# Performance work log

Hardware: AMD Instinct MI355X
Metric: run time of the kernel (lower is better)

Reference implementation:

```python
import jax, jax.numpy as jnp
import numpy as np

SPARSE_SHAPE = (41, 1600, 1408)  # (D, H, W), batch_size = 1
N_VOXELS = 200000
BN_EPS = 1e-3


def _kernel_offsets():
    # 27 offsets of a 3x3x3 kernel, padding=1 -> offsets in {-1,0,1}^3
    g = np.stack(np.meshgrid(*([np.arange(-1, 2)] * 3), indexing='ij'), axis=-1)
    return jnp.asarray(g.reshape(-1, 3), dtype=jnp.int32)  # (27, 3)


def _neighbor_map(coords):
    """Submanifold rulebook: for each active voxel and each of 27 offsets,
    index of the active neighbor voxel, or N (sentinel) if inactive/out-of-bounds."""
    D, H, W = SPARSE_SHAPE
    N = coords.shape[0]
    b, z, y, x = coords[:, 0], coords[:, 1], coords[:, 2], coords[:, 3]
    flat = ((b * D + z) * H + y) * W + x  # batch_size=1
    grid = jnp.full((D * H * W,), N, dtype=jnp.int32).at[flat].set(
        jnp.arange(N, dtype=jnp.int32))
    offs = _kernel_offsets()                      # (27, 3)
    nc = coords[:, None, 1:4] + offs[None]        # (N, 27, 3)
    lim = jnp.asarray([D, H, W], dtype=jnp.int32)
    valid = jnp.all((nc >= 0) & (nc < lim), axis=-1)  # (N, 27)
    nflat = ((b[:, None] * D + nc[..., 0]) * H + nc[..., 1]) * W + nc[..., 2]
    nbr = jnp.where(valid, grid[jnp.where(valid, nflat, 0)], N)
    return nbr  # (N, 27) int32, sentinel = N


def _subm_conv(features, nbr, w):
    # gather -> batched small GEMM -> (implicit) scatter back to same voxels
    pad = jnp.concatenate(
        [features, jnp.zeros((1, features.shape[1]), features.dtype)], axis=0)
    gathered = pad[nbr]                           # (N, 27, Cin)
    return jnp.einsum('nkc,kcd->nd', gathered, w)  # (N, Cout)


def _bn_relu(x, gamma, beta):
    # BatchNorm1d in train mode over the voxel (batch) dim, eps=1e-3
    mean = x.mean(axis=0)
    var = x.var(axis=0)
    return jax.nn.relu((x - mean) * jax.lax.rsqrt(var + BN_EPS) * gamma + beta)


def setup_inputs() -> dict:
    D, H, W = SPARSE_SHAPE
    total = D * H * W
    rng = np.random.default_rng(0)
    # unique active voxel locations
    flat = np.unique(rng.integers(0, total, size=N_VOXELS + 20000))
    rng.shuffle(flat)
    flat = flat[:N_VOXELS]
    assert flat.shape[0] == N_VOXELS
    z = flat // (H * W)
    y = (flat // W) % H
    x = flat % W
    b = np.zeros_like(z)
    coords = jnp.asarray(np.stack([b, z, y, x], axis=1), dtype=jnp.int32)

    key = jax.random.key(0)
    k0, k1, k2 = jax.random.split(key, 3)
    features = jax.random.uniform(k0, (N_VOXELS, 3), dtype=jnp.float32)
    w1 = jax.random.normal(k1, (27, 3, 16), dtype=jnp.float32) * 0.1
    w2 = jax.random.normal(k2, (27, 16, 16), dtype=jnp.float32) * 0.05
    return {
        'features': features, 'coords': coords,
        'w1': w1, 'gamma1': jnp.ones(16, jnp.float32), 'beta1': jnp.zeros(16, jnp.float32),
        'w2': w2, 'gamma2': jnp.ones(16, jnp.float32), 'beta2': jnp.zeros(16, jnp.float32),
    }


def reference(features, coords, w1, gamma1, beta1, w2, gamma2, beta2):
    nbr = _neighbor_map(coords)   # shared indice_key='subm1' -> reused by both convs
    h = _bn_relu(_subm_conv(features, nbr, w1), gamma1, beta1)
    h = _bn_relu(_subm_conv(h, nbr, w2), gamma2, beta2)
    return h
```

## Files before the change

kernel.cpp:

```cpp
#include <hip/hip_runtime.h>
#include <stdint.h>

#define SPARSE_D 41
#define SPARSE_H 1600
#define SPARSE_W 1408
#define BN_EPS 0.001f

static constexpr int NYB = SPARSE_H / 2;
static constexpr int NBUCKET = SPARSE_D * NYB;
static constexpr int PCAP = 12;


__global__ void k_insert(const int* __restrict__ coords, uint32_t* __restrict__ bent, int N) {
    int n = blockIdx.x * blockDim.x + threadIdx.x;
    if (n >= N) return;
    int4 c4 = ((const int4*)coords)[n];
    int z = c4.y, y = c4.z, x = c4.w;
    int b = z * NYB + (y >> 1);
    uint32_t e = ((uint32_t)(y & 1) << 29) | ((uint32_t)x << 18) | (uint32_t)n;
    int slot = atomicAdd((int*)&bent[(size_t)b * 32], 1) + 1;
    if (slot <= 31) bent[(size_t)b * 32 + slot] = e;
}

__device__ __forceinline__ void stats_epilogue(const float acc[16],
                                               float* __restrict__ partials,
                                               float (*sred)[32]) {
    int lid = threadIdx.x & 63;
    int wid = threadIdx.x >> 6;
    #pragma unroll
    for (int d = 0; d < 16; ++d) {
        float v = acc[d];
        float v2 = v * v;
        #pragma unroll
        for (int off = 32; off; off >>= 1) {
            v += __shfl_xor(v, off);
            v2 += __shfl_xor(v2, off);
        }
        if (lid == 0) { sred[wid][d] = v; sred[wid][16 + d] = v2; }
    }
    __syncthreads();
    if (threadIdx.x < 32)
        partials[(size_t)blockIdx.x * 32 + threadIdx.x] =
            sred[0][threadIdx.x] + sred[1][threadIdx.x] +
            sred[2][threadIdx.x] + sred[3][threadIdx.x];
}

__global__ void k_build_conv1(const int* __restrict__ coords, const uint32_t* __restrict__ bent,
                              const float* __restrict__ feat, const float* __restrict__ w1,
                              int* __restrict__ pcnt, uint32_t* __restrict__ pairs,
                              float* __restrict__ h1, float* __restrict__ partials, int N) {
    __shared__ float sred[4][32];
    int n = blockIdx.x * blockDim.x + threadIdx.x;
    float acc[16];
    #pragma unroll
    for (int d = 0; d < 16; ++d) acc[d] = 0.f;
    if (n < N) {
        int4 c4 = ((const int4*)coords)[n];
        int z = c4.y, y = c4.z, x = c4.w;

        float f0 = feat[n * 3 + 0], f1 = feat[n * 3 + 1], f2 = feat[n * 3 + 2];
        const float* wd = w1 + 13 * 48;
        #pragma unroll
        for (int d = 0; d < 16; ++d)
            acc[d] = fmaf(f0, wd[d], fmaf(f1, wd[16 + d], f2 * wd[32 + d]));

        int yb0 = (y - 1) >> 1;
        uint4 q0[6];
        int bix[6], mm[6];
        #pragma unroll
        for (int p = 0; p < 6; ++p) {
            int zz = z + p / 2 - 1;
            int yb = yb0 + (p & 1);
            bool v = ((unsigned)zz < SPARSE_D) & ((unsigned)yb < NYB);
            int b = v ? (zz * NYB + yb) : 0;
            bix[p] = b;
            q0[p] = *(const uint4*)&bent[(size_t)b * 32];
            mm[p] = v ? 1 : 0;
        }

        uint32_t lpairs[PCAP];
        int cnt = 0;
        #pragma unroll
        for (int p = 0; p < 6; ++p) {
            int m = mm[p] ? min((int)q0[p].x, 31) : 0;
            int yb = yb0 + (p & 1);
            int dzk = (p / 2) * 9;
            auto scan_entry = [&](uint32_t e, int slot) {
                if (slot > m) return;
                int ey = (yb << 1) + (int)(e >> 29);
                int ex = (int)((e >> 18) & 0x7FFu);
                int dy = ey - y, dx = ex - x;
                if ((unsigned)(dy + 1) > 2u || (unsigned)(dx + 1) > 2u) return;
                uint32_t idx = e & 0x3FFFFu;
                if (idx == (uint32_t)n) return;
                int k = dzk + (dy + 1) * 3 + (dx + 1);
                if (cnt < PCAP) lpairs[cnt] = ((uint32_t)k << 18) | idx;
                ++cnt;
            };
            scan_entry(q0[p].y, 1);
            scan_entry(q0[p].z, 2);
            scan_entry(q0[p].w, 3);
            for (int w = 4; w <= m; w += 4) {
                uint4 q = *(const uint4*)&bent[(size_t)bix[p] * 32 + w];
                scan_entry(q.x, w);
                scan_entry(q.y, w + 1);
                scan_entry(q.z, w + 2);
                scan_entry(q.w, w + 3);
            }
        }
        cnt = min(cnt, PCAP);
        pcnt[n] = cnt;
        for (int c = 0; c < cnt; ++c) {
            uint32_t pr = lpairs[c];
            pairs[(size_t)c * N + n] = pr;
            int k = (int)(pr >> 18), idx = (int)(pr & 0x3FFFFu);
            float g0 = feat[idx * 3 + 0], g1 = feat[idx * 3 + 1], g2 = feat[idx * 3 + 2];
            const float* wk = w1 + k * 48;
            #pragma unroll
            for (int d = 0; d < 16; ++d)
                acc[d] = fmaf(g0, wk[d], fmaf(g1, wk[16 + d], fmaf(g2, wk[32 + d], acc[d])));
        }
        float4* o = (float4*)&h1[(size_t)n * 16];
        o[0] = make_float4(acc[0], acc[1], acc[2], acc[3]);
        o[1] = make_float4(acc[4], acc[5], acc[6], acc[7]);
        o[2] = make_float4(acc[8], acc[9], acc[10], acc[11]);
        o[3] = make_float4(acc[12], acc[13], acc[14], acc[15]);
    }
    stats_epilogue(acc, partials, sred);
}

__global__ void k_conv2(const float* __restrict__ h1, const int* __restrict__ pcnt,
                        const uint32_t* __restrict__ pairs, const float* __restrict__ w2,
                        const float* __restrict__ scsh1, float* __restrict__ out,
                        float* __restrict__ partials, int N) {
    __shared__ float sred[4][32];
    __shared__ float sc[16], sh[16];
    if (threadIdx.x < 16) { sc[threadIdx.x] = scsh1[threadIdx.x]; sh[threadIdx.x] = scsh1[16 + threadIdx.x]; }
    __syncthreads();
    int n = blockIdx.x * blockDim.x + threadIdx.x;
    float acc[16];
    #pragma unroll
    for (int d = 0; d < 16; ++d) acc[d] = 0.f;
    if (n < N) {
        float g[16];
        #pragma unroll
        for (int c = 0; c < 16; c += 4) {
            float4 t = *(const float4*)&h1[(size_t)n * 16 + c];
            g[c]     = fmaxf(fmaf(t.x, sc[c],     sh[c]),     0.f);
            g[c + 1] = fmaxf(fmaf(t.y, sc[c + 1], sh[c + 1]), 0.f);
            g[c + 2] = fmaxf(fmaf(t.z, sc[c + 2], sh[c + 2]), 0.f);
            g[c + 3] = fmaxf(fmaf(t.w, sc[c + 3], sh[c + 3]), 0.f);
        }
        {
            const float* w = w2 + 13 * 256;
            #pragma unroll
            for (int c = 0; c < 16; ++c)
                #pragma unroll
                for (int d = 0; d < 16; ++d)
                    acc[d] = fmaf(g[c], w[c * 16 + d], acc[d]);
        }
        int m = min(pcnt[n], PCAP);
        for (int cc = 0; cc < m; ++cc) {
            uint32_t pr = pairs[(size_t)cc * N + n];
            int k = (int)(pr >> 18), idx = (int)(pr & 0x3FFFFu);
            #pragma unroll
            for (int c = 0; c < 16; c += 4) {
                float4 t = *(const float4*)&h1[(size_t)idx * 16 + c];
                g[c]     = fmaxf(fmaf(t.x, sc[c],     sh[c]),     0.f);
                g[c + 1] = fmaxf(fmaf(t.y, sc[c + 1], sh[c + 1]), 0.f);
                g[c + 2] = fmaxf(fmaf(t.z, sc[c + 2], sh[c + 2]), 0.f);
                g[c + 3] = fmaxf(fmaf(t.w, sc[c + 3], sh[c + 3]), 0.f);
            }
            const float* wk = w2 + k * 256;
            #pragma unroll
            for (int c = 0; c < 16; ++c)
                #pragma unroll
                for (int d = 0; d < 16; ++d)
                    acc[d] = fmaf(g[c], wk[c * 16 + d], acc[d]);
        }
        float4* o = (float4*)&out[(size_t)n * 16];
        o[0] = make_float4(acc[0], acc[1], acc[2], acc[3]);
        o[1] = make_float4(acc[4], acc[5], acc[6], acc[7]);
        o[2] = make_float4(acc[8], acc[9], acc[10], acc[11]);
        o[3] = make_float4(acc[12], acc[13], acc[14], acc[15]);
    }
    stats_epilogue(acc, partials, sred);
}

__global__ void k_finalize(const float* __restrict__ partials, int nb,
                           const float* __restrict__ gamma, const float* __restrict__ beta,
                           float* __restrict__ scsh, float invN) {
    __shared__ float red[32][33];
    int ch = threadIdx.x & 31;
    int rg = threadIdx.x >> 5;
    float s0 = 0.f, s1 = 0.f, s2 = 0.f, s3 = 0.f;
    int j = rg;
    for (; j + 96 < nb; j += 128) {
        s0 += partials[(size_t)(j      ) * 32 + ch];
        s1 += partials[(size_t)(j + 32 ) * 32 + ch];
        s2 += partials[(size_t)(j + 64 ) * 32 + ch];
        s3 += partials[(size_t)(j + 96 ) * 32 + ch];
    }
    for (; j < nb; j += 32) s0 += partials[(size_t)j * 32 + ch];
    red[rg][ch] = (s0 + s1) + (s2 + s3);
    __syncthreads();
    if (threadIdx.x < 32) {
        float t = 0.f;
        #pragma unroll
        for (int r = 0; r < 32; ++r) t += red[r][threadIdx.x];
        red[0][threadIdx.x] = t;
    }
    __syncthreads();
    if (threadIdx.x < 16) {
        int d = threadIdx.x;
        float mean = red[0][d] * invN;
        float var = red[0][16 + d] * invN - mean * mean;
        float s2c = gamma[d] * rsqrtf(var + BN_EPS);
        scsh[d] = s2c;
        scsh[16 + d] = beta[d] - mean * s2c;
    }
}

__global__ void k_bnrelu4(float* __restrict__ x, const float* __restrict__ scsh, int nvec) {
    __shared__ float sc[16], sh[16];
    if (threadIdx.x < 16) { sc[threadIdx.x] = scsh[threadIdx.x]; sh[threadIdx.x] = scsh[16 + threadIdx.x]; }
    __syncthreads();
    int i = blockIdx.x * blockDim.x + threadIdx.x;
    if (i < nvec) {
        float4 v = ((float4*)x)[i];
        int c0 = (i & 3) * 4;
        v.x = fmaxf(fmaf(v.x, sc[c0 + 0], sh[c0 + 0]), 0.f);
        v.y = fmaxf(fmaf(v.y, sc[c0 + 1], sh[c0 + 1]), 0.f);
        v.z = fmaxf(fmaf(v.z, sc[c0 + 2], sh[c0 + 2]), 0.f);
        v.w = fmaxf(fmaf(v.w, sc[c0 + 3], sh[c0 + 3]), 0.f);
        ((float4*)x)[i] = v;
    }
}

extern "C" void kernel_launch(void* const* d_in, const int* in_sizes, int n_in,
                              void* d_out, int out_size, void* d_ws, size_t ws_size,
                              hipStream_t stream) {
    const float* feat   = (const float*)d_in[0];
    const int*   coords = (const int*)d_in[1];
    const float* w1     = (const float*)d_in[2];
    const float* gamma1 = (const float*)d_in[3];
    const float* beta1  = (const float*)d_in[4];
    const float* w2     = (const float*)d_in[5];
    const float* gamma2 = (const float*)d_in[6];
    const float* beta2  = (const float*)d_in[7];
    float* out = (float*)d_out;
    const int N = in_sizes[0] / 3;

    const int T = 256;
    const int nb = (N + T - 1) / T;
    const int nvec = N * 16 / 4;
    const int nbv = (nvec + T - 1) / T;

    char* ws = (char*)d_ws;
    size_t off = 0;
    uint32_t* bent = (uint32_t*)(ws + off);  off += (size_t)NBUCKET * 32 * 4;
    int* pcnt = (int*)(ws + off);            off += ((size_t)N * 4 + 63) & ~(size_t)63;
    uint32_t* pairs = (uint32_t*)(ws + off); off += (size_t)PCAP * N * 4;
    float* h1 = (float*)(ws + off);          off += (size_t)N * 16 * 4;
    float* partials = (float*)(ws + off);    off += ((size_t)nb * 32 * 4 + 63) & ~(size_t)63;
    float* stats = (float*)(ws + off);

    hipMemsetAsync(bent, 0, (size_t)NBUCKET * 32 * 4, stream);
    k_insert<<<nb, T, 0, stream>>>(coords, bent, N);
    k_build_conv1<<<nb, T, 0, stream>>>(coords, bent, feat, w1, pcnt, pairs, h1, partials, N);
    k_finalize<<<1, 1024, 0, stream>>>(partials, nb, gamma1, beta1, stats, 1.f / (float)N);
    k_conv2<<<nb, T, 0, stream>>>(h1, pcnt, pairs, w2, stats, out, partials, N);
    k_finalize<<<1, 1024, 0, stream>>>(partials, nb, gamma2, beta2, stats + 32, 1.f / (float)N);
    k_bnrelu4<<<nbv, T, 0, stream>>>(out, stats + 32, nvec);
}
```

Before: 154.5 us.

## Fuse second BN finalize into apply kernel, pack pair count, stage outputs via LDS

The second finalize kernel is folded into the final BN+ReLU kernel. Each of its 128 persistent blocks now reduces the partials redundantly and then applies the result with a grid-stride loop, which removes one launch. The per-voxel pair count is packed into the top bits of the first pair word, dropping the separate pcnt array and one load. h1 and out writes, plus the self-row read of h1 in conv2, go through a shared-memory staging buffer so global accesses are fully coalesced float4s. In exchange it adds 16KB of LDS per block and extra barriers, and h1 is padded to a whole number of blocks.

```diff
diff --git a/kernel.cpp b/kernel.cpp
--- a/kernel.cpp
+++ b/kernel.cpp
@@ -45,11 +45,48 @@
             sred[2][threadIdx.x] + sred[3][threadIdx.x];
 }
 
+__device__ __forceinline__ void reduce_scsh(const float* __restrict__ partials, int nbp,
+                                            const float* __restrict__ gamma,
+                                            const float* __restrict__ beta,
+                                            float invN, float (*red)[33],
+                                            float* __restrict__ scsh) {
+    int ch = threadIdx.x & 31;
+    int rg = threadIdx.x >> 5;
+    float s0 = 0.f, s1 = 0.f, s2 = 0.f, s3 = 0.f;
+    int j = rg;
+    for (; j + 24 < nbp; j += 32) {
+        s0 += partials[(size_t)(j     ) * 32 + ch];
+        s1 += partials[(size_t)(j +  8) * 32 + ch];
+        s2 += partials[(size_t)(j + 16) * 32 + ch];
+        s3 += partials[(size_t)(j + 24) * 32 + ch];
+    }
+    for (; j < nbp; j += 8) s0 += partials[(size_t)j * 32 + ch];
+    red[rg][ch] = (s0 + s1) + (s2 + s3);
+    __syncthreads();
+    if (threadIdx.x < 32) {
+        float t = 0.f;
+        #pragma unroll
+        for (int r = 0; r < 8; ++r) t += red[r][threadIdx.x];
+        red[0][threadIdx.x] = t;
+    }
+    __syncthreads();
+    if (threadIdx.x < 16) {
+        int d = threadIdx.x;
+        float mean = red[0][d] * invN;
+        float var  = red[0][16 + d] * invN - mean * mean;
+        float sc = gamma[d] * rsqrtf(var + BN_EPS);
+        scsh[d] = sc;
+        scsh[16 + d] = beta[d] - mean * sc;
+    }
+    __syncthreads();
+}
+
 __global__ void k_build_conv1(const int* __restrict__ coords, const uint32_t* __restrict__ bent,
                               const float* __restrict__ feat, const float* __restrict__ w1,
-                              int* __restrict__ pcnt, uint32_t* __restrict__ pairs,
+                              uint32_t* __restrict__ pairs,
                               float* __restrict__ h1, float* __restrict__ partials, int N) {
     __shared__ float sred[4][32];
+    __shared__ float4 stage[256 * 4];
     int n = blockIdx.x * blockDim.x + threadIdx.x;
     float acc[16];
     #pragma unroll
@@ -109,10 +146,10 @@
             }
         }
         cnt = min(cnt, PCAP);
-        pcnt[n] = cnt;
+        pairs[n] = ((uint32_t)cnt << 24) | (cnt ? (lpairs[0] & 0xFFFFFFu) : 0u);
+        for (int c = 1; c < cnt; ++c) pairs[(size_t)c * N + n] = lpairs[c];
         for (int c = 0; c < cnt; ++c) {
             uint32_t pr = lpairs[c];
-            pairs[(size_t)c * N + n] = pr;
             int k = (int)(pr >> 18), idx = (int)(pr & 0x3FFFFu);
             float g0 = feat[idx * 3 + 0], g1 = feat[idx * 3 + 1], g2 = feat[idx * 3 + 2];
             const float* wk = w1 + k * 48;
@@ -120,22 +157,71 @@
             for (int d = 0; d < 16; ++d)
                 acc[d] = fmaf(g0, wk[d], fmaf(g1, wk[16 + d], fmaf(g2, wk[32 + d], acc[d])));
         }
-        float4* o = (float4*)&h1[(size_t)n * 16];
-        o[0] = make_float4(acc[0], acc[1], acc[2], acc[3]);
-        o[1] = make_float4(acc[4], acc[5], acc[6], acc[7]);
-        o[2] = make_float4(acc[8], acc[9], acc[10], acc[11]);
-        o[3] = make_float4(acc[12], acc[13], acc[14], acc[15]);
-    }
+    }
+    #pragma unroll
+    for (int r = 0; r < 4; ++r)
+        stage[threadIdx.x * 4 + r] = make_float4(acc[r * 4], acc[r * 4 + 1],
+                                                 acc[r * 4 + 2], acc[r * 4 + 3]);
+    __syncthreads();
+    {
+        float4* o4 = (float4*)h1;
+        size_t base = (size_t)blockIdx.x * 1024;
+        #pragma unroll
+        for (int r = 0; r < 4; ++r)
+            o4[base + r * 256 + threadIdx.x] = stage[r * 256 + threadIdx.x];
+    }
+    __syncthreads();
     stats_epilogue(acc, partials, sred);
 }
 
-__global__ void k_conv2(const float* __restrict__ h1, const int* __restrict__ pcnt,
-                        const uint32_t* __restrict__ pairs, const float* __restrict__ w2,
-                        const float* __restrict__ scsh1, float* __restrict__ out,
-                        float* __restrict__ partials, int N) {
+__global__ void k_finalize(const float* __restrict__ partials, int nb,
+                           const float* __restrict__ gamma, const float* __restrict__ beta,
+                           float* __restrict__ scsh, float invN) {
+    __shared__ float red[32][33];
+    int ch = threadIdx.x & 31;
+    int rg = threadIdx.x >> 5;
+    float s0 = 0.f, s1 = 0.f, s2 = 0.f, s3 = 0.f;
+    int j = rg;
+    for (; j + 96 < nb; j += 128) {
+        s0 += partials[(size_t)(j      ) * 32 + ch];
+        s1 += partials[(size_t)(j + 32 ) * 32 + ch];
+        s2 += partials[(size_t)(j + 64 ) * 32 + ch];
+        s3 += partials[(size_t)(j + 96 ) * 32 + ch];
+    }
+    for (; j < nb; j += 32) s0 += partials[(size_t)j * 32 + ch];
+    red[rg][ch] = (s0 + s1) + (s2 + s3);
+    __syncthreads();
+    if (threadIdx.x < 32) {
+        float t = 0.f;
+        #pragma unroll
+        for (int r = 0; r < 32; ++r) t += red[r][threadIdx.x];
+        red[0][threadIdx.x] = t;
+    }
+    __syncthreads();
+    if (threadIdx.x < 16) {
+        int d = threadIdx.x;
+        float mean = red[0][d] * invN;
+        float var = red[0][16 + d] * invN - mean * mean;
+        float s2c = gamma[d] * rsqrtf(var + BN_EPS);
+        scsh[d] = s2c;
+        scsh[16 + d] = beta[d] - mean * s2c;
+    }
+}
+
+__global__ void k_conv2(const float* __restrict__ h1, const uint32_t* __restrict__ pairs,
+                        const float* __restrict__ w2, const float* __restrict__ scsh1,
+                        float* __restrict__ out, float* __restrict__ partials, int N) {
     __shared__ float sred[4][32];
+    __shared__ float4 stage[256 * 4];
     __shared__ float sc[16], sh[16];
     if (threadIdx.x < 16) { sc[threadIdx.x] = scsh1[threadIdx.x]; sh[threadIdx.x] = scsh1[16 + threadIdx.x]; }
+    {
+        const float4* i4 = (const float4*)h1;
+        size_t base = (size_t)blockIdx.x * 1024;
+        #pragma unroll
+        for (int r = 0; r < 4; ++r)
+            stage[r * 256 + threadIdx.x] = i4[base + r * 256 + threadIdx.x];
+    }
     __syncthreads();
     int n = blockIdx.x * blockDim.x + threadIdx.x;
     float acc[16];
@@ -144,12 +230,12 @@
     if (n < N) {
         float g[16];
         #pragma unroll
-        for (int c = 0; c < 16; c += 4) {
-            float4 t = *(const float4*)&h1[(size_t)n * 16 + c];
-            g[c]     = fmaxf(fmaf(t.x, sc[c],     sh[c]),     0.f);
-            g[c + 1] = fmaxf(fmaf(t.y, sc[c + 1], sh[c + 1]), 0.f);
-            g[c + 2] = fmaxf(fmaf(t.z, sc[c + 2], sh[c + 2]), 0.f);
-            g[c + 3] = fmaxf(fmaf(t.w, sc[c + 3], sh[c + 3]), 0.f);
+        for (int cb = 0; cb < 4; ++cb) {
+            float4 t = stage[threadIdx.x * 4 + cb];
+            g[cb * 4 + 0] = fmaxf(fmaf(t.x, sc[cb * 4 + 0], sh[cb * 4 + 0]), 0.f);
+            g[cb * 4 + 1] = fmaxf(fmaf(t.y, sc[cb * 4 + 1], sh[cb * 4 + 1]), 0.f);
+            g[cb * 4 + 2] = fmaxf(fmaf(t.z, sc[cb * 4 + 2], sh[cb * 4 + 2]), 0.f);
+            g[cb * 4 + 3] = fmaxf(fmaf(t.w, sc[cb * 4 + 3], sh[cb * 4 + 3]), 0.f);
         }
         {
             const float* w = w2 + 13 * 256;
@@ -159,10 +245,12 @@
                 for (int d = 0; d < 16; ++d)
                     acc[d] = fmaf(g[c], w[c * 16 + d], acc[d]);
         }
-        int m = min(pcnt[n], PCAP);
+        uint32_t p0 = pairs[n];
+        int m = (int)(p0 >> 24);
+        uint32_t pr = p0 & 0xFFFFFFu;
         for (int cc = 0; cc < m; ++cc) {
-            uint32_t pr = pairs[(size_t)cc * N + n];
-            int k = (int)(pr >> 18), idx = (int)(pr & 0x3FFFFu);
+            if (cc > 0) pr = pairs[(size_t)cc * N + n];
+            int k = (int)((pr >> 18) & 0x1Fu), idx = (int)(pr & 0x3FFFFu);
             #pragma unroll
             for (int c = 0; c < 16; c += 4) {
                 float4 t = *(const float4*)&h1[(size_t)idx * 16 + c];
@@ -178,62 +266,41 @@
                 for (int d = 0; d < 16; ++d)
                     acc[d] = fmaf(g[c], wk[c * 16 + d], acc[d]);
         }
-        float4* o = (float4*)&out[(size_t)n * 16];
-        o[0] = make_float4(acc[0], acc[1], acc[2], acc[3]);
-        o[1] = make_float4(acc[4], acc[5], acc[6], acc[7]);
-        o[2] = make_float4(acc[8], acc[9], acc[10], acc[11]);
-        o[3] = make_float4(acc[12], acc[13], acc[14], acc[15]);
-    }
+    }
+    #pragma unroll
+    for (int r = 0; r < 4; ++r)
+        stage[threadIdx.x * 4 + r] = make_float4(acc[r * 4], acc[r * 4 + 1],
+                                                 acc[r * 4 + 2], acc[r * 4 + 3]);
+    __syncthreads();
+    {
+        float4* o4 = (float4*)out;
+        size_t base = (size_t)blockIdx.x * 1024;
+        int lim = N * 4;
+        #pragma unroll
+        for (int r = 0; r < 4; ++r) {
+            size_t gi = base + r * 256 + threadIdx.x;
+            if (gi < (size_t)lim) o4[gi] = stage[r * 256 + threadIdx.x];
+        }
+    }
+    __syncthreads();
     stats_epilogue(acc, partials, sred);
 }
 
-__global__ void k_finalize(const float* __restrict__ partials, int nb,
-                           const float* __restrict__ gamma, const float* __restrict__ beta,
-                           float* __restrict__ scsh, float invN) {
-    __shared__ float red[32][33];
-    int ch = threadIdx.x & 31;
-    int rg = threadIdx.x >> 5;
-    float s0 = 0.f, s1 = 0.f, s2 = 0.f, s3 = 0.f;
-    int j = rg;
-    for (; j + 96 < nb; j += 128) {
-        s0 += partials[(size_t)(j      ) * 32 + ch];
-        s1 += partials[(size_t)(j + 32 ) * 32 + ch];
-        s2 += partials[(size_t)(j + 64 ) * 32 + ch];
-        s3 += partials[(size_t)(j + 96 ) * 32 + ch];
-    }
-    for (; j < nb; j += 32) s0 += partials[(size_t)j * 32 + ch];
-    red[rg][ch] = (s0 + s1) + (s2 + s3);
-    __syncthreads();
-    if (threadIdx.x < 32) {
-        float t = 0.f;
-        #pragma unroll
-        for (int r = 0; r < 32; ++r) t += red[r][threadIdx.x];
-        red[0][threadIdx.x] = t;
-    }
-    __syncthreads();
-    if (threadIdx.x < 16) {
-        int d = threadIdx.x;
-        float mean = red[0][d] * invN;
-        float var = red[0][16 + d] * invN - mean * mean;
-        float s2c = gamma[d] * rsqrtf(var + BN_EPS);
-        scsh[d] = s2c;
-        scsh[16 + d] = beta[d] - mean * s2c;
-    }
-}
-
-__global__ void k_bnrelu4(float* __restrict__ x, const float* __restrict__ scsh, int nvec) {
-    __shared__ float sc[16], sh[16];
-    if (threadIdx.x < 16) { sc[threadIdx.x] = scsh[threadIdx.x]; sh[threadIdx.x] = scsh[16 + threadIdx.x]; }
-    __syncthreads();
-    int i = blockIdx.x * blockDim.x + threadIdx.x;
-    if (i < nvec) {
-        float4 v = ((float4*)x)[i];
+__global__ void k_bnrelu(float* __restrict__ out, const float* __restrict__ partials2,
+                         int nbp, const float* __restrict__ gamma2,
+                         const float* __restrict__ beta2, float invN, int nvec) {
+    __shared__ float red[8][33];
+    __shared__ float scsh[32];
+    reduce_scsh(partials2, nbp, gamma2, beta2, invN, red, scsh);
+    int stride = gridDim.x * blockDim.x;
+    for (int i = blockIdx.x * blockDim.x + threadIdx.x; i < nvec; i += stride) {
+        float4 v = ((float4*)out)[i];
         int c0 = (i & 3) * 4;
-        v.x = fmaxf(fmaf(v.x, sc[c0 + 0], sh[c0 + 0]), 0.f);
-        v.y = fmaxf(fmaf(v.y, sc[c0 + 1], sh[c0 + 1]), 0.f);
-        v.z = fmaxf(fmaf(v.z, sc[c0 + 2], sh[c0 + 2]), 0.f);
-        v.w = fmaxf(fmaf(v.w, sc[c0 + 3], sh[c0 + 3]), 0.f);
-        ((float4*)x)[i] = v;
+        v.x = fmaxf(fmaf(v.x, scsh[c0 + 0], scsh[16 + c0 + 0]), 0.f);
+        v.y = fmaxf(fmaf(v.y, scsh[c0 + 1], scsh[16 + c0 + 1]), 0.f);
+        v.z = fmaxf(fmaf(v.z, scsh[c0 + 2], scsh[16 + c0 + 2]), 0.f);
+        v.w = fmaxf(fmaf(v.w, scsh[c0 + 3], scsh[16 + c0 + 3]), 0.f);
+        ((float4*)out)[i] = v;
     }
 }
 
@@ -254,22 +321,21 @@
     const int T = 256;
     const int nb = (N + T - 1) / T;
     const int nvec = N * 16 / 4;
-    const int nbv = (nvec + T - 1) / T;
+    const float invN = 1.f / (float)N;
 
     char* ws = (char*)d_ws;
     size_t off = 0;
     uint32_t* bent = (uint32_t*)(ws + off);  off += (size_t)NBUCKET * 32 * 4;
-    int* pcnt = (int*)(ws + off);            off += ((size_t)N * 4 + 63) & ~(size_t)63;
     uint32_t* pairs = (uint32_t*)(ws + off); off += (size_t)PCAP * N * 4;
-    float* h1 = (float*)(ws + off);          off += (size_t)N * 16 * 4;
-    float* partials = (float*)(ws + off);    off += ((size_t)nb * 32 * 4 + 63) & ~(size_t)63;
+    float* h1 = (float*)(ws + off);          off += (size_t)(nb * T) * 16 * 4;
+    float* partials1 = (float*)(ws + off);   off += ((size_t)nb * 32 * 4 + 63) & ~(size_t)63;
+    float* partials2 = (float*)(ws + off);   off += ((size_t)nb * 32 * 4 + 63) & ~(size_t)63;
     float* stats = (float*)(ws + off);
 
     hipMemsetAsync(bent, 0, (size_t)NBUCKET * 32 * 4, stream);
     k_insert<<<nb, T, 0, stream>>>(coords, bent, N);
-    k_build_conv1<<<nb, T, 0, stream>>>(coords, bent, feat, w1, pcnt, pairs, h1, partials, N);
-    k_finalize<<<1, 1024, 0, stream>>>(partials, nb, gamma1, beta1, stats, 1.f / (float)N);
-    k_conv2<<<nb, T, 0, stream>>>(h1, pcnt, pairs, w2, stats, out, partials, N);
-    k_finalize<<<1, 1024, 0, stream>>>(partials, nb, gamma2, beta2, stats + 32, 1.f / (float)N);
-    k_bnrelu4<<<nbv, T, 0, stream>>>(out, stats + 32, nvec);
-}
+    k_build_conv1<<<nb, T, 0, stream>>>(coords, bent, feat, w1, pairs, h1, partials1, N);
+    k_finalize<<<1, 1024, 0, stream>>>(partials1, nb, gamma1, beta1, stats, invN);
+    k_conv2<<<nb, T, 0, stream>>>(h1, pairs, w2, stats, out, partials2, N);
+    k_bnrelu<<<128, T, 0, stream>>>(out, partials2, nb, gamma2, beta2, invN, nvec);
+}
```

After: 163.7 us. +5.9%, slower.
